# Optimization experiments

Hardware: AMD Instinct MI355X
Metric: run time of the kernel (lower is better)

The kernel has to match this reference:

```python
import jax, jax.numpy as jnp
import numpy as np

N_HEAD = 16
NEG = -1e9

def setup_inputs() -> dict:
    key = jax.random.key(0)
    k1, k2, k3 = jax.random.split(key, 3)
    B, S, NX = 8, 1024, 1024
    x = jax.random.normal(k1, (B, S, NX), dtype=jnp.float32)
    w_attn = jax.random.normal(k2, (NX, 3 * NX), dtype=jnp.float32) * 0.02
    b_attn = jnp.zeros((3 * NX,), dtype=jnp.float32)
    w_proj = jax.random.normal(k3, (NX, NX), dtype=jnp.float32) * 0.02
    b_proj = jnp.zeros((NX,), dtype=jnp.float32)
    return {"x": x, "w_attn": w_attn, "b_attn": b_attn, "w_proj": w_proj, "b_proj": b_proj}

def reference(x, w_attn, b_attn, w_proj, b_proj):
    B, S, NX = x.shape
    H = N_HEAD
    D = NX // H
    qkv = x @ w_attn + b_attn                      # [B,S,3*NX]
    q, k, v = jnp.split(qkv, 3, axis=-1)           # each [B,S,NX]
    q = q.reshape(B, S, H, D)
    k = k.reshape(B, S, H, D)
    v = v.reshape(B, S, H, D)
    # scores with scale (scale=True -> divide by sqrt(head_dim))
    w = jnp.einsum('bqhd,bkhd->bhqk', q, k) / jnp.sqrt(jnp.float32(D))
    tril = jnp.tril(jnp.ones((S, S), dtype=w.dtype))  # causal mask buffer
    w = w * tril + NEG * (1.0 - tril)
    w = jax.nn.softmax(w, axis=-1)                 # dropout is identity at eval
    a = jnp.einsum('bhqk,bkhd->bqhd', w, v)        # [B,S,H,D]
    a = a.reshape(B, S, NX)
    a = a @ w_proj + b_proj
    return a
```

## Files before the change

### kernel.cpp

```cpp
#include <hip/hip_runtime.h>
#include <hip/hip_bf16.h>
#include <stdint.h>

typedef __bf16 bf16x8 __attribute__((ext_vector_type(8)));
typedef float  f32x4  __attribute__((ext_vector_type(4)));
typedef float  f32x16 __attribute__((ext_vector_type(16)));

#define BARRIER() asm volatile("s_barrier" ::: "memory")
#define VMCNT(n)  asm volatile("s_waitcnt vmcnt(" #n ")" ::: "memory")
#define LGKM0()   asm volatile("s_waitcnt lgkmcnt(0)" ::: "memory")
#define SCHED0()  __builtin_amdgcn_sched_barrier(0)

__device__ __forceinline__ void gload_lds16(const void* g, void* l) {
  __builtin_amdgcn_global_load_lds(
      (const __attribute__((address_space(1))) unsigned int*)g,
      (__attribute__((address_space(3))) unsigned int*)l, 16, 0, 0);
}

__global__ void k_cast(const float* __restrict__ in, __bf16* __restrict__ out, int n4) {
  int i = blockIdx.x * blockDim.x + threadIdx.x;
  if (i >= n4) return;
  float4 v = reinterpret_cast<const float4*>(in)[i];
  union { __bf16 h[4]; uint64_t u; } c;
  c.h[0] = (__bf16)v.x; c.h[1] = (__bf16)v.y; c.h[2] = (__bf16)v.z; c.h[3] = (__bf16)v.w;
  *reinterpret_cast<uint64_t*>(out + 4l * i) = c.u;
}

__global__ void k_transpose_cast(const float* __restrict__ in, __bf16* __restrict__ out,
                                 int R, int C) {
  __shared__ float t[32][33];
  const int tx = threadIdx.x & 31, ty = threadIdx.x >> 5;
  const int c0 = blockIdx.x * 32, r0 = blockIdx.y * 32;
#pragma unroll
  for (int rr = 0; rr < 4; ++rr)
    t[ty * 4 + rr][tx] = in[(long)(r0 + ty * 4 + rr) * C + c0 + tx];
  __syncthreads();
#pragma unroll
  for (int rr = 0; rr < 4; ++rr)
    out[(long)(c0 + ty * 4 + rr) * R + r0 + tx] = (__bf16)t[tx][ty * 4 + rr];
}

template <int MODE>
__launch_bounds__(512, 2)
__global__ void k_gemm_p(const __bf16* __restrict__ A, const __bf16* __restrict__ Bt,
                         const float* __restrict__ bias, int M, int N, int K, int NB,
                         __bf16* __restrict__ qo, __bf16* __restrict__ ko,
                         __bf16* __restrict__ vo, float* __restrict__ fo) {
  __shared__ __bf16 lds[3][24576];
  const int tid = threadIdx.x;
  const int l = tid & 63;
  const int w = tid >> 6;
  const int lm = l & 15, lq = l >> 4;
  const int wm = w >> 2, wn = w & 3;
  const int nwg = gridDim.x;
  const int wg = (blockIdx.x & 7) * (nwg >> 3) + (blockIdx.x >> 3);
  const int bm = wg / NB, bn = wg % NB;
  const int nt = K >> 6;

  const int rA = tid >> 3;
  const int scol = (((tid & 7) * 16) ^ ((rA & 7) << 4)) >> 1;
  long a_off[4], b_off[2];
#pragma unroll
  for (int li = 0; li < 4; ++li) a_off[li] = (long)(bm * 256 + li * 64 + rA) * K + scol;
#pragma unroll
  for (int li = 0; li < 2; ++li) b_off[li] = (long)(bn * 128 + li * 64 + rA) * K + scol;

#define STAGE_A(buf, t) { \
    gload_lds16(A + a_off[0] + (long)(t) * 64, &lds[buf][tid * 8]); \
    gload_lds16(A + a_off[1] + (long)(t) * 64, &lds[buf][4096 + tid * 8]); \
    gload_lds16(A + a_off[2] + (long)(t) * 64, &lds[buf][8192 + tid * 8]); \
    gload_lds16(A + a_off[3] + (long)(t) * 64, &lds[buf][12288 + tid * 8]); }
#define STAGE_B(buf, t) { \
    gload_lds16(Bt + b_off[0] + (long)(t) * 64, &lds[buf][16384 + tid * 8]); \
    gload_lds16(Bt + b_off[1] + (long)(t) * 64, &lds[buf][20480 + tid * 8]); }

  const int aswz = (lm & 7) << 4;
  const int cofs0 = ((0 * 64 + lq * 16) ^ aswz) >> 1;
  const int cofs1 = ((1 * 64 + lq * 16) ^ aswz) >> 1;
  const int arow = wm * 128 + lm;
  const int brow = wn * 32 + lm;

  f32x4 acc[8][2] = {};

  STAGE_A(0, 0); STAGE_B(0, 0);
  STAGE_A(1, 1); STAGE_B(1, 1);
  VMCNT(6); BARRIER();

  for (int t = 0; t < nt; ++t) {
    const int cb = t % 3;
    const __bf16* Lb = lds[cb];
    bf16x8 bf[2][2], af[4][2];
#pragma unroll
    for (int nj = 0; nj < 2; ++nj) {
      bf[nj][0] = *(const bf16x8*)&Lb[16384 + (brow + nj * 16) * 64 + cofs0];
      bf[nj][1] = *(const bf16x8*)&Lb[16384 + (brow + nj * 16) * 64 + cofs1];
    }
#pragma unroll
    for (int mi = 0; mi < 4; ++mi) {
      af[mi][0] = *(const bf16x8*)&Lb[(arow + mi * 16) * 64 + cofs0];
      af[mi][1] = *(const bf16x8*)&Lb[(arow + mi * 16) * 64 + cofs1];
    }
    if (t + 2 < nt) STAGE_A((t + 2) % 3, t + 2);
    BARRIER();
    LGKM0(); SCHED0();
    __builtin_amdgcn_s_setprio(1);
#pragma unroll
    for (int ks = 0; ks < 2; ++ks)
#pragma unroll
      for (int mi = 0; mi < 4; ++mi)
#pragma unroll
        for (int nj = 0; nj < 2; ++nj)
          acc[mi][nj] = __builtin_amdgcn_mfma_f32_16x16x32_bf16(af[mi][ks], bf[nj][ks],
                                                                acc[mi][nj], 0, 0, 0);
    __builtin_amdgcn_s_setprio(0);
    SCHED0();
    BARRIER();
#pragma unroll
    for (int mi = 0; mi < 4; ++mi) {
      af[mi][0] = *(const bf16x8*)&Lb[(arow + (mi + 4) * 16) * 64 + cofs0];
      af[mi][1] = *(const bf16x8*)&Lb[(arow + (mi + 4) * 16) * 64 + cofs1];
    }
    if (t + 2 < nt) {
      STAGE_B((t + 2) % 3, t + 2);
      VMCNT(6);
    } else {
      VMCNT(0);
    }
    BARRIER();
    LGKM0(); SCHED0();
    __builtin_amdgcn_s_setprio(1);
#pragma unroll
    for (int ks = 0; ks < 2; ++ks)
#pragma unroll
      for (int mi = 0; mi < 4; ++mi)
#pragma unroll
        for (int nj = 0; nj < 2; ++nj)
          acc[mi + 4][nj] = __builtin_amdgcn_mfma_f32_16x16x32_bf16(af[mi][ks], bf[nj][ks],
                                                                    acc[mi + 4][nj], 0, 0, 0);
    __builtin_amdgcn_s_setprio(0);
    SCHED0();
    BARRIER();
  }

  if (MODE == 0) {
#pragma unroll
    for (int nj = 0; nj < 2; ++nj) {
      const int c = bn * 128 + wn * 32 + nj * 16 + lm;
      const float bv = bias[c];
      const int which = c >> 10, cc = c & 1023, hh = cc >> 6, d = cc & 63;
#pragma unroll
      for (int mi = 0; mi < 8; ++mi)
#pragma unroll
        for (int i = 0; i < 4; ++i) {
          const int r = bm * 256 + wm * 128 + mi * 16 + lq * 4 + i;
          const int b = r >> 10, s_ = r & 1023;
          float fv = acc[mi][nj][i] + bv;
          if (which == 0) fv *= 0.125f;
          const __bf16 v = (__bf16)fv;
          const long hb = (long)(b * 16 + hh);
          if (which == 0)      qo[(hb * 1024 + s_) * 64 + d] = v;
          else if (which == 1) ko[(hb * 1024 + s_) * 64 + d] = v;
          else                 vo[(hb * 64 + d) * 1024 + s_] = v;
        }
    }
  } else {
#pragma unroll
    for (int nj = 0; nj < 2; ++nj) {
      const int c = bn * 128 + wn * 32 + nj * 16 + lm;
      const float bv = bias[c];
#pragma unroll
      for (int mi = 0; mi < 8; ++mi)
#pragma unroll
        for (int i = 0; i < 4; ++i) {
          const int r = bm * 256 + wm * 128 + mi * 16 + lq * 4 + i;
          fo[(long)r * N + c] = acc[mi][nj][i] + bv;
        }
    }
  }
#undef STAGE_A
#undef STAGE_B
}

__device__ __forceinline__ void sm_pv(f32x16& st, float& m, float& s,
                                      f32x16& o0, f32x16& o1,
                                      const bf16x8 vf[2][2],
                                      int qbw, int k0, bool diag, int lm, int hi) {
  if (diag) {
    const int q = qbw + lm;
#pragma unroll
    for (int r = 0; r < 16; ++r) {
      const int key = k0 + (r & 3) + 8 * (r >> 2) + 4 * hi;
      if (key > q) st[r] = -__builtin_inff();
    }
  }
  float tm = st[0];
#pragma unroll
  for (int r = 1; r < 16; ++r) tm = fmaxf(tm, st[r]);
  tm = fmaxf(tm, __shfl_xor(tm, 32));
  if (!__all(tm <= m + 8.f)) {
    const float mn = fmaxf(m, tm);
    const float fac = __expf(m - mn);
    m = mn;
    s *= fac;
#pragma unroll
    for (int r = 0; r < 16; ++r) {
      const int qr = (r & 3) + 8 * (r >> 2) + 4 * hi;
      const float fr = __int_as_float(
          __builtin_amdgcn_ds_bpermute(qr * 4, __float_as_int(fac)));
      o0[r] *= fr; o1[r] *= fr;
    }
  }
  float p[16], ts = 0.f;
#pragma unroll
  for (int r = 0; r < 16; ++r) { p[r] = __expf(st[r] - m); ts += p[r]; }
  ts += __shfl_xor(ts, 32);
  s += ts;
  unsigned int w8[8];
#pragma unroll
  for (int t = 0; t < 8; ++t) {
    union { __bf16 hh[2]; unsigned int u; } pk;
    pk.hh[0] = (__bf16)p[2 * t]; pk.hh[1] = (__bf16)p[2 * t + 1];
    w8[t] = pk.u;
  }
  const unsigned int e0 = __shfl_xor(hi ? w8[0] : w8[2], 32);
  const unsigned int e1 = __shfl_xor(hi ? w8[1] : w8[3], 32);
  const unsigned int e2 = __shfl_xor(hi ? w8[4] : w8[6], 32);
  const unsigned int e3 = __shfl_xor(hi ? w8[5] : w8[7], 32);
  union { unsigned int wd[4]; bf16x8 v; } pa0, pa1;
  if (hi) {
    pa0.wd[0] = e0;    pa0.wd[1] = e1;    pa0.wd[2] = w8[2]; pa0.wd[3] = w8[3];
    pa1.wd[0] = e2;    pa1.wd[1] = e3;    pa1.wd[2] = w8[6]; pa1.wd[3] = w8[7];
  } else {
    pa0.wd[0] = w8[0]; pa0.wd[1] = w8[1]; pa0.wd[2] = e0;    pa0.wd[3] = e1;
    pa1.wd[0] = w8[4]; pa1.wd[1] = w8[5]; pa1.wd[2] = e2;    pa1.wd[3] = e3;
  }
#pragma unroll
  for (int t = 0; t < 2; ++t) {
    const bf16x8 pa = t ? pa1.v : pa0.v;
    o0 = __builtin_amdgcn_mfma_f32_32x32x16_bf16(pa, vf[t][0], o0, 0, 0, 0);
    o1 = __builtin_amdgcn_mfma_f32_32x32x16_bf16(pa, vf[t][1], o1, 0, 0, 0);
  }
}

__device__ __forceinline__ void attn_write(const f32x16& o0, const f32x16& o1, float s,
                                           __bf16* __restrict__ ob,
                                           int b, int h, int qbw, int lm, int hi) {
  const float invs = 1.f / s;
#pragma unroll
  for (int r = 0; r < 16; ++r) {
    const int qr = (r & 3) + 8 * (r >> 2) + 4 * hi;
    const float inv = __int_as_float(
        __builtin_amdgcn_ds_bpermute(qr * 4, __float_as_int(invs)));
    const long row = (long)(b * 1024 + qbw + qr) * 1024 + h * 64;
    ob[row + lm]      = (__bf16)(o0[r] * inv);
    ob[row + 32 + lm] = (__bf16)(o1[r] * inv);
  }
}

__global__ void k_attn(const __bf16* __restrict__ qb_, const __bf16* __restrict__ kb,
                       const __bf16* __restrict__ vtb, __bf16* __restrict__ ob) {
  const int l = threadIdx.x & 63, w = threadIdx.x >> 6;
  const int lm = l & 31, hi = l >> 5;
  const int bh = blockIdx.y, b = bh >> 4, h = bh & 15;
  const int wi = blockIdx.x * 4 + w;
  const __bf16* Q  = qb_ + (long)bh * 65536;
  const __bf16* Kh = kb  + (long)bh * 65536;
  const __bf16* Vt = vtb + (long)bh * 65536;

  const int qbA = wi * 32,        ntA = wi + 1;
  const int qbB = (31 - wi) * 32, ntB = 32 - wi;

  bf16x8 qfA[4], qfB[4];
#pragma unroll
  for (int ds = 0; ds < 4; ++ds) {
    qfA[ds] = *(const bf16x8*)(Q + (long)(qbA + lm) * 64 + ds * 16 + hi * 8);
    qfB[ds] = *(const bf16x8*)(Q + (long)(qbB + lm) * 64 + ds * 16 + hi * 8);
  }

  f32x16 oA0 = {}, oA1 = {}, oB0 = {}, oB1 = {};
  float mA = -__builtin_inff(), sA = 0.f;
  float mB = -__builtin_inff(), sB = 0.f;

  for (int kt = 0; kt < ntB; ++kt) {
    const int k0 = kt * 32;
    const bool actA = (kt < ntA);
    bf16x8 kf[4];
#pragma unroll
    for (int ds = 0; ds < 4; ++ds)
      kf[ds] = *(const bf16x8*)(Kh + (long)(k0 + lm) * 64 + ds * 16 + hi * 8);
    f32x16 stA = {}, stB = {};
#pragma unroll
    for (int ds = 0; ds < 4; ++ds)
      stB = __builtin_amdgcn_mfma_f32_32x32x16_bf16(kf[ds], qfB[ds], stB, 0, 0, 0);
    if (actA) {
#pragma unroll
      for (int ds = 0; ds < 4; ++ds)
        stA = __builtin_amdgcn_mfma_f32_32x32x16_bf16(kf[ds], qfA[ds], stA, 0, 0, 0);
    }
    bf16x8 vf[2][2];
#pragma unroll
    for (int t = 0; t < 2; ++t) {
      vf[t][0] = *(const bf16x8*)(Vt + (long)lm * 1024 + k0 + t * 16 + hi * 8);
      vf[t][1] = *(const bf16x8*)(Vt + (long)(32 + lm) * 1024 + k0 + t * 16 + hi * 8);
    }
    if (actA) sm_pv(stA, mA, sA, oA0, oA1, vf, qbA, k0, kt == ntA - 1, lm, hi);
    sm_pv(stB, mB, sB, oB0, oB1, vf, qbB, k0, kt == ntB - 1, lm, hi);
  }
  attn_write(oA0, oA1, sA, ob, b, h, qbA, lm, hi);
  attn_write(oB0, oB1, sB, ob, b, h, qbB, lm, hi);
}

extern "C" void kernel_launch(void* const* d_in, const int* in_sizes, int n_in,
                              void* d_out, int out_size, void* d_ws, size_t ws_size,
                              hipStream_t stream) {
  const float* x      = (const float*)d_in[0];
  const float* w_attn = (const float*)d_in[1];
  const float* b_attn = (const float*)d_in[2];
  const float* w_proj = (const float*)d_in[3];
  const float* b_proj = (const float*)d_in[4];
  float* out = (float*)d_out;

  char* ws = (char*)d_ws;
  const size_t SZ_XBF = (size_t)8192 * 1024 * 2;
  __bf16* x_bf = (__bf16*)ws;  ws += SZ_XBF;
  __bf16* wat  = (__bf16*)ws;  ws += (size_t)3072 * 1024 * 2;
  __bf16* wpt  = (__bf16*)ws;  ws += (size_t)1024 * 1024 * 2;
  __bf16* qb   = (__bf16*)ws;  ws += SZ_XBF;
  __bf16* kb   = (__bf16*)ws;  ws += SZ_XBF;
  __bf16* vtb  = (__bf16*)ws;  ws += SZ_XBF;
  __bf16* obf  = (__bf16*)ws;  ws += SZ_XBF;

  k_cast<<<8192, 256, 0, stream>>>(x, x_bf, 2097152);
  k_transpose_cast<<<dim3(96, 32), 256, 0, stream>>>(w_attn, wat, 1024, 3072);
  k_transpose_cast<<<dim3(32, 32), 256, 0, stream>>>(w_proj, wpt, 1024, 1024);
  k_gemm_p<0><<<768, 512, 0, stream>>>(x_bf, wat, b_attn, 8192, 3072, 1024, 24,
                                       qb, kb, vtb, nullptr);
  k_attn<<<dim3(4, 128), 256, 0, stream>>>(qb, kb, vtb, obf);
  k_gemm_p<1><<<256, 512, 0, stream>>>(obf, wpt, b_proj, 8192, 1024, 1024, 8,
                                       nullptr, nullptr, nullptr, out);
}
```

Baseline: 331.8 us.

## Process attention q-tiles sequentially and remap blocks so heads share an XCD

Each wave now handles its two causal q-tiles one after another instead of interleaving them in one loop. This drops the duplicated Q fragments and accumulators, so register pressure falls and occupancy may rise, but K/V tiles are now loaded twice per wave. The grid is also flattened, and block IDs are remapped so the four blocks of one (batch, head) land on the same XCD (bid & 7), which is meant to improve L2 reuse of K/V. The trade-off is less K/V reuse within a wave and serialized causal work per wave.

```diff
diff --git a/kernel.cpp b/kernel.cpp
--- a/kernel.cpp
+++ b/kernel.cpp
@@ -181,70 +181,88 @@
 #undef STAGE_B
 }
 
-__device__ __forceinline__ void sm_pv(f32x16& st, float& m, float& s,
-                                      f32x16& o0, f32x16& o1,
-                                      const bf16x8 vf[2][2],
-                                      int qbw, int k0, bool diag, int lm, int hi) {
-  if (diag) {
-    const int q = qbw + lm;
-#pragma unroll
-    for (int r = 0; r < 16; ++r) {
-      const int key = k0 + (r & 3) + 8 * (r >> 2) + 4 * hi;
-      if (key > q) st[r] = -__builtin_inff();
+__device__ __forceinline__ void attn_qtile(const __bf16* __restrict__ Q,
+                                           const __bf16* __restrict__ Kh,
+                                           const __bf16* __restrict__ Vt,
+                                           __bf16* __restrict__ ob,
+                                           int b, int h, int qbw, int l) {
+  const int lm = l & 31, hi = l >> 5;
+
+  bf16x8 qf[4];
+#pragma unroll
+  for (int ds = 0; ds < 4; ++ds)
+    qf[ds] = *(const bf16x8*)(Q + (long)(qbw + lm) * 64 + ds * 16 + hi * 8);
+
+  f32x16 oacc0 = {}, oacc1 = {};
+  float m = -__builtin_inff(), s = 0.f;
+
+  const int ntiles = (qbw >> 5) + 1;
+  for (int kt = 0; kt < ntiles; ++kt) {
+    const int k0 = kt * 32;
+    f32x16 st = {};
+#pragma unroll
+    for (int ds = 0; ds < 4; ++ds) {
+      bf16x8 kf = *(const bf16x8*)(Kh + (long)(k0 + lm) * 64 + ds * 16 + hi * 8);
+      st = __builtin_amdgcn_mfma_f32_32x32x16_bf16(kf, qf[ds], st, 0, 0, 0);
+    }
+    if (kt == ntiles - 1) {
+      const int q = qbw + lm;
+#pragma unroll
+      for (int r = 0; r < 16; ++r) {
+        const int key = k0 + (r & 3) + 8 * (r >> 2) + 4 * hi;
+        if (key > q) st[r] = -__builtin_inff();
+      }
+    }
+    float tm = st[0];
+#pragma unroll
+    for (int r = 1; r < 16; ++r) tm = fmaxf(tm, st[r]);
+    tm = fmaxf(tm, __shfl_xor(tm, 32));
+    if (!__all(tm <= m + 8.f)) {
+      const float mn = fmaxf(m, tm);
+      const float fac = __expf(m - mn);
+      m = mn;
+      s *= fac;
+#pragma unroll
+      for (int r = 0; r < 16; ++r) {
+        const int qr = (r & 3) + 8 * (r >> 2) + 4 * hi;
+        const float fr = __int_as_float(
+            __builtin_amdgcn_ds_bpermute(qr * 4, __float_as_int(fac)));
+        oacc0[r] *= fr; oacc1[r] *= fr;
+      }
+    }
+    float p[16], ts = 0.f;
+#pragma unroll
+    for (int r = 0; r < 16; ++r) { p[r] = __expf(st[r] - m); ts += p[r]; }
+    ts += __shfl_xor(ts, 32);
+    s += ts;
+    unsigned int w8[8];
+#pragma unroll
+    for (int t = 0; t < 8; ++t) {
+      union { __bf16 hh[2]; unsigned int u; } pk;
+      pk.hh[0] = (__bf16)p[2 * t]; pk.hh[1] = (__bf16)p[2 * t + 1];
+      w8[t] = pk.u;
+    }
+    const unsigned int e0 = __shfl_xor(hi ? w8[0] : w8[2], 32);
+    const unsigned int e1 = __shfl_xor(hi ? w8[1] : w8[3], 32);
+    const unsigned int e2 = __shfl_xor(hi ? w8[4] : w8[6], 32);
+    const unsigned int e3 = __shfl_xor(hi ? w8[5] : w8[7], 32);
+    union { unsigned int wd[4]; bf16x8 v; } pa0, pa1;
+    if (hi) {
+      pa0.wd[0] = e0;    pa0.wd[1] = e1;    pa0.wd[2] = w8[2]; pa0.wd[3] = w8[3];
+      pa1.wd[0] = e2;    pa1.wd[1] = e3;    pa1.wd[2] = w8[6]; pa1.wd[3] = w8[7];
+    } else {
+      pa0.wd[0] = w8[0]; pa0.wd[1] = w8[1]; pa0.wd[2] = e0;    pa0.wd[3] = e1;
+      pa1.wd[0] = w8[4]; pa1.wd[1] = w8[5]; pa1.wd[2] = e2;    pa1.wd[3] = e3;
+    }
+#pragma unroll
+    for (int t = 0; t < 2; ++t) {
+      const bf16x8 pa = t ? pa1.v : pa0.v;
+      bf16x8 vf0 = *(const bf16x8*)(Vt + (long)lm * 1024 + k0 + t * 16 + hi * 8);
+      bf16x8 vf1 = *(const bf16x8*)(Vt + (long)(32 + lm) * 1024 + k0 + t * 16 + hi * 8);
+      oacc0 = __builtin_amdgcn_mfma_f32_32x32x16_bf16(pa, vf0, oacc0, 0, 0, 0);
+      oacc1 = __builtin_amdgcn_mfma_f32_32x32x16_bf16(pa, vf1, oacc1, 0, 0, 0);
     }
   }
-  float tm = st[0];
-#pragma unroll
-  for (int r = 1; r < 16; ++r) tm = fmaxf(tm, st[r]);
-  tm = fmaxf(tm, __shfl_xor(tm, 32));
-  if (!__all(tm <= m + 8.f)) {
-    const float mn = fmaxf(m, tm);
-    const float fac = __expf(m - mn);
-    m = mn;
-    s *= fac;
-#pragma unroll
-    for (int r = 0; r < 16; ++r) {
-      const int qr = (r & 3) + 8 * (r >> 2) + 4 * hi;
-      const float fr = __int_as_float(
-          __builtin_amdgcn_ds_bpermute(qr * 4, __float_as_int(fac)));
-      o0[r] *= fr; o1[r] *= fr;
-    }
-  }
-  float p[16], ts = 0.f;
-#pragma unroll
-  for (int r = 0; r < 16; ++r) { p[r] = __expf(st[r] - m); ts += p[r]; }
-  ts += __shfl_xor(ts, 32);
-  s += ts;
-  unsigned int w8[8];
-#pragma unroll
-  for (int t = 0; t < 8; ++t) {
-    union { __bf16 hh[2]; unsigned int u; } pk;
-    pk.hh[0] = (__bf16)p[2 * t]; pk.hh[1] = (__bf16)p[2 * t + 1];
-    w8[t] = pk.u;
-  }
-  const unsigned int e0 = __shfl_xor(hi ? w8[0] : w8[2], 32);
-  const unsigned int e1 = __shfl_xor(hi ? w8[1] : w8[3], 32);
-  const unsigned int e2 = __shfl_xor(hi ? w8[4] : w8[6], 32);
-  const unsigned int e3 = __shfl_xor(hi ? w8[5] : w8[7], 32);
-  union { unsigned int wd[4]; bf16x8 v; } pa0, pa1;
-  if (hi) {
-    pa0.wd[0] = e0;    pa0.wd[1] = e1;    pa0.wd[2] = w8[2]; pa0.wd[3] = w8[3];
-    pa1.wd[0] = e2;    pa1.wd[1] = e3;    pa1.wd[2] = w8[6]; pa1.wd[3] = w8[7];
-  } else {
-    pa0.wd[0] = w8[0]; pa0.wd[1] = w8[1]; pa0.wd[2] = e0;    pa0.wd[3] = e1;
-    pa1.wd[0] = w8[4]; pa1.wd[1] = w8[5]; pa1.wd[2] = e2;    pa1.wd[3] = e3;
-  }
-#pragma unroll
-  for (int t = 0; t < 2; ++t) {
-    const bf16x8 pa = t ? pa1.v : pa0.v;
-    o0 = __builtin_amdgcn_mfma_f32_32x32x16_bf16(pa, vf[t][0], o0, 0, 0, 0);
-    o1 = __builtin_amdgcn_mfma_f32_32x32x16_bf16(pa, vf[t][1], o1, 0, 0, 0);
-  }
-}
-
-__device__ __forceinline__ void attn_write(const f32x16& o0, const f32x16& o1, float s,
-                                           __bf16* __restrict__ ob,
-                                           int b, int h, int qbw, int lm, int hi) {
   const float invs = 1.f / s;
 #pragma unroll
   for (int r = 0; r < 16; ++r) {
@@ -252,62 +270,25 @@
     const float inv = __int_as_float(
         __builtin_amdgcn_ds_bpermute(qr * 4, __float_as_int(invs)));
     const long row = (long)(b * 1024 + qbw + qr) * 1024 + h * 64;
-    ob[row + lm]      = (__bf16)(o0[r] * inv);
-    ob[row + 32 + lm] = (__bf16)(o1[r] * inv);
+    ob[row + lm]      = (__bf16)(oacc0[r] * inv);
+    ob[row + 32 + lm] = (__bf16)(oacc1[r] * inv);
   }
 }
 
 __global__ void k_attn(const __bf16* __restrict__ qb_, const __bf16* __restrict__ kb,
                        const __bf16* __restrict__ vtb, __bf16* __restrict__ ob) {
   const int l = threadIdx.x & 63, w = threadIdx.x >> 6;
-  const int lm = l & 31, hi = l >> 5;
-  const int bh = blockIdx.y, b = bh >> 4, h = bh & 15;
-  const int wi = blockIdx.x * 4 + w;
+  const int bid = blockIdx.x;
+  const int xcd = bid & 7, slot = bid >> 3;
+  const int bh = xcd + 8 * (slot >> 2);
+  const int j = slot & 3;
+  const int wi = j * 4 + w;
+  const int b = bh >> 4, h = bh & 15;
   const __bf16* Q  = qb_ + (long)bh * 65536;
   const __bf16* Kh = kb  + (long)bh * 65536;
   const __bf16* Vt = vtb + (long)bh * 65536;
-
-  const int qbA = wi * 32,        ntA = wi + 1;
-  const int qbB = (31 - wi) * 32, ntB = 32 - wi;
-
-  bf16x8 qfA[4], qfB[4];
-#pragma unroll
-  for (int ds = 0; ds < 4; ++ds) {
-    qfA[ds] = *(const bf16x8*)(Q + (long)(qbA + lm) * 64 + ds * 16 + hi * 8);
-    qfB[ds] = *(const bf16x8*)(Q + (long)(qbB + lm) * 64 + ds * 16 + hi * 8);
-  }
-
-  f32x16 oA0 = {}, oA1 = {}, oB0 = {}, oB1 = {};
-  float mA = -__builtin_inff(), sA = 0.f;
-  float mB = -__builtin_inff(), sB = 0.f;
-
-  for (int kt = 0; kt < ntB; ++kt) {
-    const int k0 = kt * 32;
-    const bool actA = (kt < ntA);
-    bf16x8 kf[4];
-#pragma unroll
-    for (int ds = 0; ds < 4; ++ds)
-      kf[ds] = *(const bf16x8*)(Kh + (long)(k0 + lm) * 64 + ds * 16 + hi * 8);
-    f32x16 stA = {}, stB = {};
-#pragma unroll
-    for (int ds = 0; ds < 4; ++ds)
-      stB = __builtin_amdgcn_mfma_f32_32x32x16_bf16(kf[ds], qfB[ds], stB, 0, 0, 0);
-    if (actA) {
-#pragma unroll
-      for (int ds = 0; ds < 4; ++ds)
-        stA = __builtin_amdgcn_mfma_f32_32x32x16_bf16(kf[ds], qfA[ds], stA, 0, 0, 0);
-    }
-    bf16x8 vf[2][2];
-#pragma unroll
-    for (int t = 0; t < 2; ++t) {
-      vf[t][0] = *(const bf16x8*)(Vt + (long)lm * 1024 + k0 + t * 16 + hi * 8);
-      vf[t][1] = *(const bf16x8*)(Vt + (long)(32 + lm) * 1024 + k0 + t * 16 + hi * 8);
-    }
-    if (actA) sm_pv(stA, mA, sA, oA0, oA1, vf, qbA, k0, kt == ntA - 1, lm, hi);
-    sm_pv(stB, mB, sB, oB0, oB1, vf, qbB, k0, kt == ntB - 1, lm, hi);
-  }
-  attn_write(oA0, oA1, sA, ob, b, h, qbA, lm, hi);
-  attn_write(oB0, oB1, sB, ob, b, h, qbB, lm, hi);
+  attn_qtile(Q, Kh, Vt, ob, b, h, wi * 32, l);
+  attn_qtile(Q, Kh, Vt, ob, b, h, (31 - wi) * 32, l);
 }
 
 extern "C" void kernel_launch(void* const* d_in, const int* in_sizes, int n_in,
@@ -335,7 +316,7 @@
   k_transpose_cast<<<dim3(32, 32), 256, 0, stream>>>(w_proj, wpt, 1024, 1024);
   k_gemm_p<0><<<768, 512, 0, stream>>>(x_bf, wat, b_attn, 8192, 3072, 1024, 24,
                                        qb, kb, vtb, nullptr);
-  k_attn<<<dim3(4, 128), 256, 0, stream>>>(qb, kb, vtb, obf);
+  k_attn<<<512, 256, 0, stream>>>(qb, kb, vtb, obf);
   k_gemm_p<1><<<256, 512, 0, stream>>>(obf, wpt, b_proj, 8192, 1024, 1024, 8,
                                        nullptr, nullptr, nullptr, out);
 }
```

Result: faster. 287.5 us (-13.3%).
